# Kernel tuning notes

Hardware: AMD Instinct MI355X
Metric: run time of the kernel (lower is better)

## Reference

```python
import jax, jax.numpy as jnp
import numpy as np

B, L, H, K = 16, 512, 1024, 8192

def setup_inputs() -> dict:
    key = jax.random.key(0)
    k1, k2 = jax.random.split(key)
    inputs = jax.random.normal(k1, (B, L, H), dtype=jnp.float32)
    masks = jnp.ones((B, L), dtype=bool)
    # xavier_uniform for Linear(hidden_size, labels_num): weight [K, H]
    limit = float(np.sqrt(6.0 / (H + K)))
    W = jax.random.uniform(k2, (K, H), dtype=jnp.float32, minval=-limit, maxval=limit)
    return {"inputs": inputs, "masks": masks, "W": W}

def reference(inputs, masks, W):
    # scores: [B, K, L] = (inputs @ W.T).transpose(1,2)
    scores = jnp.einsum('blh,kh->bkl', inputs, W)
    scores = jnp.where(masks[:, None, :], scores, -jnp.inf)
    attn = jax.nn.softmax(scores, axis=-1)          # softmax over L
    return jnp.einsum('bkl,blh->bkh', attn, inputs)  # [B, K, H]
```

## Files before the change

### kernel.cpp

```cpp
#include <hip/hip_runtime.h>
#include <stdint.h>

#define BN 16
#define LN 512
#define HN 1024
#define KN 8192
#define TK 64
#define NTHREADS 512

typedef float  f32x4  __attribute__((ext_vector_type(4)));
typedef __bf16 bf16x8 __attribute__((ext_vector_type(8)));
typedef __bf16 bf16x4 __attribute__((ext_vector_type(4)));

__device__ __forceinline__ void cp16(const void* g, void* l) {
  __builtin_amdgcn_global_load_lds(
      (const __attribute__((address_space(1))) unsigned int*)g,
      (__attribute__((address_space(3))) unsigned int*)l, 16, 0, 0);
}

__global__ void cvt_w(const float* __restrict__ W, __bf16* __restrict__ Wb) {
  const size_t i = (size_t)blockIdx.x * blockDim.x + threadIdx.x;
  const float4 v = ((const float4*)W)[i];
  bf16x4 o; o[0] = (__bf16)v.x; o[1] = (__bf16)v.y; o[2] = (__bf16)v.z; o[3] = (__bf16)v.w;
  ((bf16x4*)Wb)[i] = o;
}

__global__ void trans_x(const float* __restrict__ X, __bf16* __restrict__ Xb,
                        __bf16* __restrict__ Xt) {
  __shared__ __bf16 T[64][72];
  const int b  = blockIdx.y;
  const int l0 = (blockIdx.x & 7) * 64;
  const int h0 = (blockIdx.x >> 3) * 64;
  const int t  = threadIdx.x;
  #pragma unroll
  for (int it = 0; it < 4; ++it) {
    const int idx = it * 256 + t;
    const int lr = idx >> 4, hc = (idx & 15) << 2;
    const float4 v = *(const float4*)(X + ((size_t)b * LN + l0 + lr) * HN + h0 + hc);
    bf16x4 o; o[0] = (__bf16)v.x; o[1] = (__bf16)v.y; o[2] = (__bf16)v.z; o[3] = (__bf16)v.w;
    *(bf16x4*)(Xb + ((size_t)b * LN + l0 + lr) * HN + h0 + hc) = o;
    *(bf16x4*)&T[lr][hc] = o;
  }
  __syncthreads();
  #pragma unroll
  for (int it = 0; it < 4; ++it) {
    const int idx = it * 256 + t;
    const int hr = idx >> 4, lg = (idx & 15) << 2;
    bf16x4 o;
    o[0] = T[lg + 0][hr]; o[1] = T[lg + 1][hr];
    o[2] = T[lg + 2][hr]; o[3] = T[lg + 3][hr];
    *(bf16x4*)(Xt + ((size_t)b * HN + h0 + hr) * LN + l0 + lg) = o;
  }
}

#define AT_LDA 520

struct __align__(16) PhaseMem {
  __bf16 attn[TK][AT_LDA];
  __bf16 stage[512 * 64];
  __bf16 wt[64 * 64];
  float redM[8][TK];
  float redS[8][TK];
  float Mf[TK];
  float Sinv[TK];
};
union SMem {
  PhaseMem p;
  float osm[TK * 516];
};

__global__ __launch_bounds__(NTHREADS, 1)
void mlattn_fused2(const __bf16* __restrict__ Wb, const __bf16* __restrict__ Xb,
                   const __bf16* __restrict__ Xt, const int* __restrict__ Mk,
                   float* __restrict__ out) {
  __shared__ SMem sm;
  const int t    = threadIdx.x;
  const int wv   = t >> 6;
  const int lane = t & 63;
  const int q    = lane >> 4;
  const int c    = lane & 15;
  const int b    = blockIdx.y;
  const int k0   = blockIdx.x * TK;
  const __bf16* Xbb = Xb + (size_t)b * LN * HN;
  const __bf16* Xtb = Xt + (size_t)b * HN * LN;
  const f32x4 fzero = {0.f, 0.f, 0.f, 0.f};

  f32x4 acc[4][4];
  #pragma unroll
  for (int mt = 0; mt < 4; ++mt)
    #pragma unroll
    for (int nt = 0; nt < 4; ++nt) acc[mt][nt] = fzero;

  const int lw0 = wv * 64;

  for (int h0 = 0; h0 < HN; h0 += 64) {
    {
      const int row = t >> 3, jj = t & 7;
      cp16(Wb + (size_t)(k0 + row) * HN + h0 + ((jj ^ (row & 7)) << 3),
           &sm.p.wt[t * 8]);
    }
    #pragma unroll
    for (int i = 0; i < 8; ++i) {
      const int s = i * 512 + t;
      const int row = s >> 3, jj = s & 7;
      cp16(Xbb + (size_t)row * HN + h0 + ((jj ^ (row & 7)) << 3),
           &sm.p.stage[s * 8]);
    }
    __syncthreads();
    #pragma unroll
    for (int ks = 0; ks < 2; ++ks) {
      bf16x8 aF[4], bF[4];
      #pragma unroll
      for (int mt = 0; mt < 4; ++mt) {
        const int r = mt * 16 + c;
        aF[mt] = *(const bf16x8*)&sm.p.wt[r * 64 + (((ks * 4 + q) ^ (c & 7)) << 3)];
      }
      #pragma unroll
      for (int nt = 0; nt < 4; ++nt) {
        const int r = lw0 + nt * 16 + c;
        bF[nt] = *(const bf16x8*)&sm.p.stage[r * 64 + (((ks * 4 + q) ^ (c & 7)) << 3)];
      }
      #pragma unroll
      for (int mt = 0; mt < 4; ++mt)
        #pragma unroll
        for (int nt = 0; nt < 4; ++nt)
          acc[mt][nt] = __builtin_amdgcn_mfma_f32_16x16x32_bf16(aF[mt], bF[nt], acc[mt][nt], 0, 0, 0);
    }
    __syncthreads();
  }

  #pragma unroll
  for (int nt = 0; nt < 4; ++nt) {
    const int m = Mk[b * LN + lw0 + nt * 16 + c];
    if (!m) {
      #pragma unroll
      for (int mt = 0; mt < 4; ++mt)
        #pragma unroll
        for (int r = 0; r < 4; ++r) acc[mt][nt][r] = -1e30f;
    }
  }
  float pm[4][4];
  #pragma unroll
  for (int mt = 0; mt < 4; ++mt)
    #pragma unroll
    for (int r = 0; r < 4; ++r)
      pm[mt][r] = fmaxf(fmaxf(acc[mt][0][r], acc[mt][1][r]), fmaxf(acc[mt][2][r], acc[mt][3][r]));
  #pragma unroll
  for (int off = 1; off < 16; off <<= 1)
    #pragma unroll
    for (int mt = 0; mt < 4; ++mt)
      #pragma unroll
      for (int r = 0; r < 4; ++r)
        pm[mt][r] = fmaxf(pm[mt][r], __shfl_xor(pm[mt][r], off, 64));
  if (c == 0) {
    #pragma unroll
    for (int mt = 0; mt < 4; ++mt)
      #pragma unroll
      for (int r = 0; r < 4; ++r) sm.p.redM[wv][mt * 16 + q * 4 + r] = pm[mt][r];
  }
  __syncthreads();
  if (t < TK) {
    float m = sm.p.redM[0][t];
    #pragma unroll
    for (int w = 1; w < 8; ++w) m = fmaxf(m, sm.p.redM[w][t]);
    sm.p.Mf[t] = m;
  }
  __syncthreads();

  float ps[4][4];
  #pragma unroll
  for (int mt = 0; mt < 4; ++mt)
    #pragma unroll
    for (int r = 0; r < 4; ++r) {
      const float M = sm.p.Mf[mt * 16 + q * 4 + r];
      float s = 0.f;
      #pragma unroll
      for (int nt = 0; nt < 4; ++nt) {
        const float e = __expf(acc[mt][nt][r] - M);
        acc[mt][nt][r] = e;
        s += e;
      }
      ps[mt][r] = s;
    }
  #pragma unroll
  for (int off = 1; off < 16; off <<= 1)
    #pragma unroll
    for (int mt = 0; mt < 4; ++mt)
      #pragma unroll
      for (int r = 0; r < 4; ++r) ps[mt][r] += __shfl_xor(ps[mt][r], off, 64);
  if (c == 0) {
    #pragma unroll
    for (int mt = 0; mt < 4; ++mt)
      #pragma unroll
      for (int r = 0; r < 4; ++r) sm.p.redS[wv][mt * 16 + q * 4 + r] = ps[mt][r];
  }
  __syncthreads();
  if (t < TK) {
    float s = 0.f;
    #pragma unroll
    for (int w = 0; w < 8; ++w) s += sm.p.redS[w][t];
    sm.p.Sinv[t] = 1.f / s;
  }
  __syncthreads();

  #pragma unroll
  for (int mt = 0; mt < 4; ++mt)
    #pragma unroll
    for (int r = 0; r < 4; ++r) {
      const int row = mt * 16 + q * 4 + r;
      const float inv = sm.p.Sinv[row];
      #pragma unroll
      for (int nt = 0; nt < 4; ++nt)
        sm.p.attn[row][lw0 + nt * 16 + c] = (__bf16)(acc[mt][nt][r] * inv);
    }

  const int wM = wv >> 2;
  const int wN = wv & 3;
  f32x4 acc2[2][16];
  #pragma unroll
  for (int i = 0; i < 2; ++i)
    #pragma unroll
    for (int j = 0; j < 16; ++j) acc2[i][j] = fzero;

  for (int lc = 0; lc < 8; ++lc) {
    const int l0c = lc * 64;
    #pragma unroll
    for (int hh = 0; hh < 2; ++hh) {
      #pragma unroll
      for (int i = 0; i < 8; ++i) {
        const int s = i * 512 + t;
        const int row = s >> 3, jj = s & 7;
        cp16(Xtb + (size_t)(hh * 512 + row) * LN + l0c + ((jj ^ (row & 7)) << 3),
             &sm.p.stage[s * 8]);
      }
      __syncthreads();
      #pragma unroll
      for (int ks = 0; ks < 2; ++ks) {
        bf16x8 aF2[2], bF2[8];
        #pragma unroll
        for (int mt = 0; mt < 2; ++mt)
          aF2[mt] = *(const bf16x8*)&sm.p.attn[wM * 32 + mt * 16 + c][l0c + ks * 32 + q * 8];
        #pragma unroll
        for (int nt = 0; nt < 8; ++nt) {
          const int r = wN * 128 + nt * 16 + c;
          bF2[nt] = *(const bf16x8*)&sm.p.stage[r * 64 + (((ks * 4 + q) ^ (c & 7)) << 3)];
        }
        #pragma unroll
        for (int mt = 0; mt < 2; ++mt)
          #pragma unroll
          for (int nt = 0; nt < 8; ++nt)
            acc2[mt][hh * 8 + nt] =
                __builtin_amdgcn_mfma_f32_16x16x32_bf16(aF2[mt], bF2[nt], acc2[mt][hh * 8 + nt], 0, 0, 0);
      }
      __syncthreads();
    }
  }

  float* outb = out + ((size_t)b * KN + k0) * HN;
  #pragma unroll
  for (int hh = 0; hh < 2; ++hh) {
    if (hh) __syncthreads();
    #pragma unroll
    for (int mt = 0; mt < 2; ++mt)
      #pragma unroll
      for (int nt = 0; nt < 8; ++nt) {
        const int hl = wN * 128 + nt * 16 + c;
        #pragma unroll
        for (int r = 0; r < 4; ++r) {
          const int krow = wM * 32 + mt * 16 + q * 4 + r;
          sm.osm[krow * 516 + hl] = acc2[mt][hh * 8 + nt][r];
        }
      }
    __syncthreads();
    #pragma unroll
    for (int i = 0; i < 16; ++i) {
      const int s = i * 512 + t;
      const int row = s >> 7, col4 = s & 127;
      *(f32x4*)(outb + (size_t)row * HN + hh * 512 + (col4 << 2)) =
          *(const f32x4*)&sm.osm[row * 516 + (col4 << 2)];
    }
  }
}

#define XT_LDA 72
#define WT_LDA 72
#define AT_LDA_O 520
#define X2_LDA 72

struct __align__(16) SMemOld {
  __bf16 attn[TK][AT_LDA_O];
  union {
    struct { __bf16 xt[LN][XT_LDA]; __bf16 wt[TK][WT_LDA]; } p1;
    __bf16 x2[512][X2_LDA];
  } u;
  float redM[8][TK];
  float redS[8][TK];
  float Mf[TK];
  float Sinv[TK];
};

__device__ __forceinline__ bf16x4 cvt4o(float4 v) {
  bf16x4 r;
  r[0] = (__bf16)v.x; r[1] = (__bf16)v.y; r[2] = (__bf16)v.z; r[3] = (__bf16)v.w;
  return r;
}

__global__ __launch_bounds__(NTHREADS, 2)
void mlattn_fused(const float* __restrict__ X, const int* __restrict__ Mk,
                  const float* __restrict__ W, float* __restrict__ out) {
  __shared__ SMemOld sm;
  const int t    = threadIdx.x;
  const int wv   = t >> 6;
  const int lane = t & 63;
  const int q    = lane >> 4;
  const int c    = lane & 15;
  const int b    = blockIdx.y;
  const int k0   = blockIdx.x * TK;
  const float* Xb = X + (size_t)b * LN * HN;
  const f32x4 fzero = {0.f, 0.f, 0.f, 0.f};

  f32x4 acc[4][4];
  #pragma unroll
  for (int mt = 0; mt < 4; ++mt)
    #pragma unroll
    for (int nt = 0; nt < 4; ++nt) acc[mt][nt] = fzero;

  const int lw0 = wv * 64;
  const int sr  = t >> 4;
  const int sc  = t & 15;

  for (int h0 = 0; h0 < HN; h0 += 64) {
    #pragma unroll
    for (int p = 0; p < 2; ++p) {
      const int row = p * 32 + sr;
      float4 v = *(const float4*)(W + (size_t)(k0 + row) * HN + h0 + sc * 4);
      *(bf16x4*)&sm.u.p1.wt[row][sc * 4] = cvt4o(v);
    }
    #pragma unroll
    for (int p = 0; p < 16; ++p) {
      const int row = p * 32 + sr;
      float4 v = *(const float4*)(Xb + (size_t)row * HN + h0 + sc * 4);
      *(bf16x4*)&sm.u.p1.xt[row][sc * 4] = cvt4o(v);
    }
    __syncthreads();
    #pragma unroll
    for (int ks = 0; ks < 2; ++ks) {
      bf16x8 aF[4], bF[4];
      #pragma unroll
      for (int mt = 0; mt < 4; ++mt)
        aF[mt] = *(const bf16x8*)&sm.u.p1.wt[mt * 16 + c][ks * 32 + q * 8];
      #pragma unroll
      for (int nt = 0; nt < 4; ++nt)
        bF[nt] = *(const bf16x8*)&sm.u.p1.xt[lw0 + nt * 16 + c][ks * 32 + q * 8];
      #pragma unroll
      for (int mt = 0; mt < 4; ++mt)
        #pragma unroll
        for (int nt = 0; nt < 4; ++nt)
          acc[mt][nt] = __builtin_amdgcn_mfma_f32_16x16x32_bf16(aF[mt], bF[nt], acc[mt][nt], 0, 0, 0);
    }
    __syncthreads();
  }

  #pragma unroll
  for (int nt = 0; nt < 4; ++nt) {
    const int m = Mk[b * LN + lw0 + nt * 16 + c];
    if (!m) {
      #pragma unroll
      for (int mt = 0; mt < 4; ++mt)
        #pragma unroll
        for (int r = 0; r < 4; ++r) acc[mt][nt][r] = -1e30f;
    }
  }

  float pm[4][4];
  #pragma unroll
  for (int mt = 0; mt < 4; ++mt)
    #pragma unroll
    for (int r = 0; r < 4; ++r)
      pm[mt][r] = fmaxf(fmaxf(acc[mt][0][r], acc[mt][1][r]), fmaxf(acc[mt][2][r], acc[mt][3][r]));
  #pragma unroll
  for (int off = 1; off < 16; off <<= 1)
    #pragma unroll
    for (int mt = 0; mt < 4; ++mt)
      #pragma unroll
      for (int r = 0; r < 4; ++r)
        pm[mt][r] = fmaxf(pm[mt][r], __shfl_xor(pm[mt][r], off, 64));
  if (c == 0) {
    #pragma unroll
    for (int mt = 0; mt < 4; ++mt)
      #pragma unroll
      for (int r = 0; r < 4; ++r) sm.redM[wv][mt * 16 + q * 4 + r] = pm[mt][r];
  }
  __syncthreads();
  if (t < TK) {
    float m = sm.redM[0][t];
    #pragma unroll
    for (int w = 1; w < 8; ++w) m = fmaxf(m, sm.redM[w][t]);
    sm.Mf[t] = m;
  }
  __syncthreads();

  float ps[4][4];
  #pragma unroll
  for (int mt = 0; mt < 4; ++mt)
    #pragma unroll
    for (int r = 0; r < 4; ++r) {
      const float M = sm.Mf[mt * 16 + q * 4 + r];
      float s = 0.f;
      #pragma unroll
      for (int nt = 0; nt < 4; ++nt) {
        const float e = __expf(acc[mt][nt][r] - M);
        acc[mt][nt][r] = e;
        s += e;
      }
      ps[mt][r] = s;
    }
  #pragma unroll
  for (int off = 1; off < 16; off <<= 1)
    #pragma unroll
    for (int mt = 0; mt < 4; ++mt)
      #pragma unroll
      for (int r = 0; r < 4; ++r) ps[mt][r] += __shfl_xor(ps[mt][r], off, 64);
  if (c == 0) {
    #pragma unroll
    for (int mt = 0; mt < 4; ++mt)
      #pragma unroll
      for (int r = 0; r < 4; ++r) sm.redS[wv][mt * 16 + q * 4 + r] = ps[mt][r];
  }
  __syncthreads();
  if (t < TK) {
    float s = 0.f;
    #pragma unroll
    for (int w = 0; w < 8; ++w) s += sm.redS[w][t];
    sm.Sinv[t] = 1.f / s;
  }
  __syncthreads();

  #pragma unroll
  for (int mt = 0; mt < 4; ++mt)
    #pragma unroll
    for (int r = 0; r < 4; ++r) {
      const int row = mt * 16 + q * 4 + r;
      const float inv = sm.Sinv[row];
      #pragma unroll
      for (int nt = 0; nt < 4; ++nt)
        sm.attn[row][lw0 + nt * 16 + c] = (__bf16)(acc[mt][nt][r] * inv);
    }

  const int wM = wv >> 2;
  const int wN = wv & 3;
  f32x4 acc2[2][16];
  #pragma unroll
  for (int i = 0; i < 2; ++i)
    #pragma unroll
    for (int j = 0; j < 16; ++j) acc2[i][j] = fzero;

  for (int lc = 0; lc < 8; ++lc) {
    const int l0c = lc * 64;
    #pragma unroll
    for (int hh = 0; hh < 2; ++hh) {
      __syncthreads();
      {
        const float* xcol = Xb + (size_t)hh * 512 + t;
        #pragma unroll
        for (int u = 0; u < 16; ++u) {
          const int l = l0c + u * 4;
          const float d0 = xcol[(size_t)(l + 0) * HN];
          const float d1 = xcol[(size_t)(l + 1) * HN];
          const float d2 = xcol[(size_t)(l + 2) * HN];
          const float d3 = xcol[(size_t)(l + 3) * HN];
          bf16x4 p;
          p[0] = (__bf16)d0; p[1] = (__bf16)d1; p[2] = (__bf16)d2; p[3] = (__bf16)d3;
          *(bf16x4*)&sm.u.x2[t][u * 4] = p;
        }
      }
      __syncthreads();
      #pragma unroll
      for (int ks = 0; ks < 2; ++ks) {
        bf16x8 aF2[2], bF2[8];
        #pragma unroll
        for (int mt = 0; mt < 2; ++mt)
          aF2[mt] = *(const bf16x8*)&sm.attn[wM * 32 + mt * 16 + c][l0c + ks * 32 + q * 8];
        #pragma unroll
        for (int nt = 0; nt < 8; ++nt)
          bF2[nt] = *(const bf16x8*)&sm.u.x2[wN * 128 + nt * 16 + c][ks * 32 + q * 8];
        #pragma unroll
        for (int mt = 0; mt < 2; ++mt)
          #pragma unroll
          for (int nt = 0; nt < 8; ++nt)
            acc2[mt][hh * 8 + nt] =
                __builtin_amdgcn_mfma_f32_16x16x32_bf16(aF2[mt], bF2[nt], acc2[mt][hh * 8 + nt], 0, 0, 0);
      }
    }
  }

  float* outb = out + ((size_t)b * KN + k0) * HN;
  #pragma unroll
  for (int mt = 0; mt < 2; ++mt) {
    #pragma unroll
    for (int j = 0; j < 16; ++j) {
      const int hh = j >> 3, nt = j & 7;
      const int h = hh * 512 + wN * 128 + nt * 16 + c;
      #pragma unroll
      for (int r = 0; r < 4; ++r) {
        const int krow = wM * 32 + mt * 16 + q * 4 + r;
        outb[(size_t)krow * HN + h] = acc2[mt][j][r];
      }
    }
  }
}

extern "C" void kernel_launch(void* const* d_in, const int* in_sizes, int n_in,
                              void* d_out, int out_size, void* d_ws, size_t ws_size,
                              hipStream_t stream) {
  (void)in_sizes; (void)n_in; (void)out_size;
  const float* X = (const float*)d_in[0];
  const int* Mk = (const int*)d_in[1];
  const float* W = (const float*)d_in[2];
  float* out = (float*)d_out;

  const size_t need = ((size_t)KN * HN + 2 * (size_t)BN * LN * HN) * sizeof(__bf16);
  if (d_ws == nullptr || ws_size < need) {
    dim3 grid(KN / TK, BN);
    mlattn_fused<<<grid, NTHREADS, 0, stream>>>(X, Mk, W, out);
    return;
  }

  __bf16* Wb = (__bf16*)d_ws;
  __bf16* Xbb = Wb + (size_t)KN * HN;
  __bf16* Xtb = Xbb + (size_t)BN * LN * HN;

  cvt_w<<<(KN * HN / 4) / 256, 256, 0, stream>>>(W, Wb);
  trans_x<<<dim3(128, BN), 256, 0, stream>>>(X, Xbb, Xtb);
  mlattn_fused2<<<dim3(KN / TK, BN), NTHREADS, 0, stream>>>(Wb, Xbb, Xtb, Mk, out);
}
```

Baseline: 1.079 ms.

## Double-buffer LDS staging in both GEMM phases to overlap loads with MFMA

Splits shared memory into separate double-buffered regions for the score GEMM (X and W tiles) and the attention-times-X GEMM (transposed X tiles). The next tile is issued with async global-to-LDS copies while MFMAs run on the current one, and the first phase-2 tile is prefetched during the softmax reductions. Phase 2 is restructured into 32 steps over 32-wide L chunks with a new XOR swizzle. This removes one barrier-separated load stall per tile, but raises LDS use to near capacity and relies on correct waitcnt placement for the async copies.

Result: faster. 1.001 ms (-7.2%).

```diff
diff --git a/kernel.cpp b/kernel.cpp
--- a/kernel.cpp
+++ b/kernel.cpp
@@ -53,20 +53,26 @@
   }
 }
 
-#define AT_LDA 520
-
-struct __align__(16) PhaseMem {
-  __bf16 attn[TK][AT_LDA];
-  __bf16 stage[512 * 64];
-  __bf16 wt[64 * 64];
+#define P2_AT_LDA 520
+
+struct __align__(16) P1Mem {
+  __bf16 xs[2][512 * 64];
+  __bf16 wt[2][64 * 64];
+};
+struct __align__(16) P2Mem {
+  __bf16 attn[TK][P2_AT_LDA];
+  __bf16 xt[2][512 * 32];
+};
+struct __align__(16) SMem {
+  union {
+    P1Mem p1;
+    P2Mem p2;
+    float osm[TK * 516];
+  } u;
   float redM[8][TK];
   float redS[8][TK];
   float Mf[TK];
   float Sinv[TK];
-};
-union SMem {
-  PhaseMem p;
-  float osm[TK * 516];
 };
 
 __global__ __launch_bounds__(NTHREADS, 1)
@@ -85,6 +91,14 @@
   const __bf16* Xtb = Xt + (size_t)b * HN * LN;
   const f32x4 fzero = {0.f, 0.f, 0.f, 0.f};
 
+  const int tr8 = t >> 3, tc8 = t & 7;
+  const int colOff1 = ((tc8 ^ (tr8 & 7)) << 3);
+  const __bf16* xsrc = Xbb + (size_t)tr8 * HN + colOff1;
+  const __bf16* wsrc = Wb + (size_t)(k0 + tr8) * HN + colOff1;
+  const int tr4 = t >> 2, tc4 = t & 3;
+  const int colOff2 = ((tc4 ^ ((t >> 3) & 3)) << 3);
+  const __bf16* tsrc = Xtb + (size_t)tr4 * LN + colOff2;
+
   f32x4 acc[4][4];
   #pragma unroll
   for (int mt = 0; mt < 4; ++mt)
@@ -93,32 +107,35 @@
 
   const int lw0 = wv * 64;
 
-  for (int h0 = 0; h0 < HN; h0 += 64) {
-    {
-      const int row = t >> 3, jj = t & 7;
-      cp16(Wb + (size_t)(k0 + row) * HN + h0 + ((jj ^ (row & 7)) << 3),
-           &sm.p.wt[t * 8]);
-    }
-    #pragma unroll
-    for (int i = 0; i < 8; ++i) {
-      const int s = i * 512 + t;
-      const int row = s >> 3, jj = s & 7;
-      cp16(Xbb + (size_t)row * HN + h0 + ((jj ^ (row & 7)) << 3),
-           &sm.p.stage[s * 8]);
-    }
-    __syncthreads();
+  {
+    cp16(wsrc, &sm.u.p1.wt[0][t * 8]);
+    #pragma unroll
+    for (int i = 0; i < 8; ++i)
+      cp16(xsrc + (size_t)i * 64 * HN, &sm.u.p1.xs[0][(i * 512 + t) * 8]);
+  }
+  __syncthreads();
+
+  int cur = 0;
+  for (int tt = 0; tt < 16; ++tt) {
+    if (tt + 1 < 16) {
+      const int h0 = (tt + 1) * 64;
+      cp16(wsrc + h0, &sm.u.p1.wt[cur ^ 1][t * 8]);
+      #pragma unroll
+      for (int i = 0; i < 8; ++i)
+        cp16(xsrc + (size_t)i * 64 * HN + h0, &sm.u.p1.xs[cur ^ 1][(i * 512 + t) * 8]);
+    }
     #pragma unroll
     for (int ks = 0; ks < 2; ++ks) {
       bf16x8 aF[4], bF[4];
       #pragma unroll
       for (int mt = 0; mt < 4; ++mt) {
         const int r = mt * 16 + c;
-        aF[mt] = *(const bf16x8*)&sm.p.wt[r * 64 + (((ks * 4 + q) ^ (c & 7)) << 3)];
+        aF[mt] = *(const bf16x8*)&sm.u.p1.wt[cur][r * 64 + (((ks * 4 + q) ^ (c & 7)) << 3)];
       }
       #pragma unroll
       for (int nt = 0; nt < 4; ++nt) {
         const int r = lw0 + nt * 16 + c;
-        bF[nt] = *(const bf16x8*)&sm.p.stage[r * 64 + (((ks * 4 + q) ^ (c & 7)) << 3)];
+        bF[nt] = *(const bf16x8*)&sm.u.p1.xs[cur][r * 64 + (((ks * 4 + q) ^ (c & 7)) << 3)];
       }
       #pragma unroll
       for (int mt = 0; mt < 4; ++mt)
@@ -127,6 +144,13 @@
           acc[mt][nt] = __builtin_amdgcn_mfma_f32_16x16x32_bf16(aF[mt], bF[nt], acc[mt][nt], 0, 0, 0);
     }
     __syncthreads();
+    cur ^= 1;
+  }
+
+  {
+    #pragma unroll
+    for (int i = 0; i < 4; ++i)
+      cp16(tsrc + (size_t)i * 128 * LN, &sm.u.p2.xt[0][(i * 512 + t) * 8]);
   }
 
   #pragma unroll
@@ -156,14 +180,14 @@
     #pragma unroll
     for (int mt = 0; mt < 4; ++mt)
       #pragma unroll
-      for (int r = 0; r < 4; ++r) sm.p.redM[wv][mt * 16 + q * 4 + r] = pm[mt][r];
+      for (int r = 0; r < 4; ++r) sm.redM[wv][mt * 16 + q * 4 + r] = pm[mt][r];
   }
   __syncthreads();
   if (t < TK) {
-    float m = sm.p.redM[0][t];
-    #pragma unroll
-    for (int w = 1; w < 8; ++w) m = fmaxf(m, sm.p.redM[w][t]);
-    sm.p.Mf[t] = m;
+    float m = sm.redM[0][t];
+    #pragma unroll
+    for (int w = 1; w < 8; ++w) m = fmaxf(m, sm.redM[w][t]);
+    sm.Mf[t] = m;
   }
   __syncthreads();
 
@@ -172,7 +196,7 @@
   for (int mt = 0; mt < 4; ++mt)
     #pragma unroll
     for (int r = 0; r < 4; ++r) {
-      const float M = sm.p.Mf[mt * 16 + q * 4 + r];
+      const float M = sm.Mf[mt * 16 + q * 4 + r];
       float s = 0.f;
       #pragma unroll
       for (int nt = 0; nt < 4; ++nt) {
@@ -192,14 +216,14 @@
     #pragma unroll
     for (int mt = 0; mt < 4; ++mt)
       #pragma unroll
-      for (int r = 0; r < 4; ++r) sm.p.redS[wv][mt * 16 + q * 4 + r] = ps[mt][r];
+      for (int r = 0; r < 4; ++r) sm.redS[wv][mt * 16 + q * 4 + r] = ps[mt][r];
   }
   __syncthreads();
   if (t < TK) {
     float s = 0.f;
     #pragma unroll
-    for (int w = 0; w < 8; ++w) s += sm.p.redS[w][t];
-    sm.p.Sinv[t] = 1.f / s;
+    for (int w = 0; w < 8; ++w) s += sm.redS[w][t];
+    sm.Sinv[t] = 1.f / s;
   }
   __syncthreads();
 
@@ -208,52 +232,50 @@
     #pragma unroll
     for (int r = 0; r < 4; ++r) {
       const int row = mt * 16 + q * 4 + r;
-      const float inv = sm.p.Sinv[row];
+      const float inv = sm.Sinv[row];
       #pragma unroll
       for (int nt = 0; nt < 4; ++nt)
-        sm.p.attn[row][lw0 + nt * 16 + c] = (__bf16)(acc[mt][nt][r] * inv);
-    }
+        sm.u.p2.attn[row][lw0 + nt * 16 + c] = (__bf16)(acc[mt][nt][r] * inv);
+    }
+  __syncthreads();
 
   const int wM = wv >> 2;
   const int wN = wv & 3;
+  const int swq8 = ((q ^ ((c >> 1) & 3)) << 3);
   f32x4 acc2[2][16];
   #pragma unroll
   for (int i = 0; i < 2; ++i)
     #pragma unroll
     for (int j = 0; j < 16; ++j) acc2[i][j] = fzero;
 
-  for (int lc = 0; lc < 8; ++lc) {
-    const int l0c = lc * 64;
-    #pragma unroll
-    for (int hh = 0; hh < 2; ++hh) {
-      #pragma unroll
-      for (int i = 0; i < 8; ++i) {
-        const int s = i * 512 + t;
-        const int row = s >> 3, jj = s & 7;
-        cp16(Xtb + (size_t)(hh * 512 + row) * LN + l0c + ((jj ^ (row & 7)) << 3),
-             &sm.p.stage[s * 8]);
-      }
-      __syncthreads();
-      #pragma unroll
-      for (int ks = 0; ks < 2; ++ks) {
-        bf16x8 aF2[2], bF2[8];
-        #pragma unroll
-        for (int mt = 0; mt < 2; ++mt)
-          aF2[mt] = *(const bf16x8*)&sm.p.attn[wM * 32 + mt * 16 + c][l0c + ks * 32 + q * 8];
-        #pragma unroll
-        for (int nt = 0; nt < 8; ++nt) {
-          const int r = wN * 128 + nt * 16 + c;
-          bF2[nt] = *(const bf16x8*)&sm.p.stage[r * 64 + (((ks * 4 + q) ^ (c & 7)) << 3)];
-        }
-        #pragma unroll
-        for (int mt = 0; mt < 2; ++mt)
-          #pragma unroll
-          for (int nt = 0; nt < 8; ++nt)
-            acc2[mt][hh * 8 + nt] =
-                __builtin_amdgcn_mfma_f32_16x16x32_bf16(aF2[mt], bF2[nt], acc2[mt][hh * 8 + nt], 0, 0, 0);
-      }
-      __syncthreads();
-    }
+  cur = 0;
+  for (int s = 0; s < 32; ++s) {
+    if (s + 1 < 32) {
+      const int sn = s + 1;
+      const __bf16* src = tsrc + (size_t)((sn & 1) * 512) * LN + ((sn >> 1) << 5);
+      #pragma unroll
+      for (int i = 0; i < 4; ++i)
+        cp16(src + (size_t)i * 128 * LN, &sm.u.p2.xt[cur ^ 1][(i * 512 + t) * 8]);
+    }
+    const int l0c = (s >> 1) << 5;
+    const int hh  = s & 1;
+    bf16x8 aF2[2], bF2[8];
+    #pragma unroll
+    for (int mt = 0; mt < 2; ++mt)
+      aF2[mt] = *(const bf16x8*)&sm.u.p2.attn[wM * 32 + mt * 16 + c][l0c + q * 8];
+    #pragma unroll
+    for (int nt = 0; nt < 8; ++nt) {
+      const int r = wN * 128 + nt * 16 + c;
+      bF2[nt] = *(const bf16x8*)&sm.u.p2.xt[cur][r * 32 + swq8];
+    }
+    #pragma unroll
+    for (int mt = 0; mt < 2; ++mt)
+      #pragma unroll
+      for (int nt = 0; nt < 8; ++nt)
+        acc2[mt][hh * 8 + nt] =
+            __builtin_amdgcn_mfma_f32_16x16x32_bf16(aF2[mt], bF2[nt], acc2[mt][hh * 8 + nt], 0, 0, 0);
+    __syncthreads();
+    cur ^= 1;
   }
 
   float* outb = out + ((size_t)b * KN + k0) * HN;
@@ -268,7 +290,7 @@
         #pragma unroll
         for (int r = 0; r < 4; ++r) {
           const int krow = wM * 32 + mt * 16 + q * 4 + r;
-          sm.osm[krow * 516 + hl] = acc2[mt][hh * 8 + nt][r];
+          sm.u.osm[krow * 516 + hl] = acc2[mt][hh * 8 + nt][r];
         }
       }
     __syncthreads();
@@ -277,7 +299,7 @@
       const int s = i * 512 + t;
       const int row = s >> 7, col4 = s & 127;
       *(f32x4*)(outb + (size_t)row * HN + hh * 512 + (col4 << 2)) =
-          *(const f32x4*)&sm.osm[row * 516 + (col4 << 2)];
+          *(const f32x4*)&sm.u.osm[row * 516 + (col4 << 2)];
     }
   }
 }
```
